# Performance work log

Hardware: AMD Instinct MI355X
Metric: run time of the kernel (lower is better)

The kernel has to match this reference:

```python
import jax, jax.numpy as jnp
import numpy as np

B, S, E, D, A = 32, 2048, 1024, 1024, 1024


def setup_inputs() -> dict:
    key = jax.random.key(0)
    k1, k2, k3, k4, k5, k6, k7, k8 = jax.random.split(key, 8)
    # Kaiming-uniform-ish init scales (values don't matter for correctness)
    def lin(kw, kb, fan_in, fan_out):
        bound = 1.0 / np.sqrt(fan_in)
        W = jax.random.uniform(kw, (fan_out, fan_in), minval=-bound, maxval=bound, dtype=jnp.float32)
        b = jax.random.uniform(kb, (fan_out,), minval=-bound, maxval=bound, dtype=jnp.float32)
        return W, b
    W_enc, b_enc = lin(k1, k2, E, A)
    W_dec, b_dec = lin(k3, k4, D, A)
    W_v, b_v = lin(k5, k6, A, 1)
    encoder_out = jax.random.normal(k7, (B, S, E), dtype=jnp.float32)
    decoder_hidden = jax.random.normal(k8, (B, D), dtype=jnp.float32)
    return {
        "encoder_out": encoder_out,
        "decoder_hidden": decoder_hidden,
        "W_enc": W_enc, "b_enc": b_enc,
        "W_dec": W_dec, "b_dec": b_dec,
        "W_v": W_v, "b_v": b_v,
    }


def reference(encoder_out, decoder_hidden, W_enc, b_enc, W_dec, b_dec, W_v, b_v):
    # encoder_proj: [B, S, A]
    encoder_proj = jnp.einsum('bse,ae->bsa', encoder_out, W_enc) + b_enc
    # decoder_proj: [B, 1, A]
    decoder_proj = (jnp.einsum('bd,ad->ba', decoder_hidden, W_dec) + b_dec)[:, None, :]
    # scores: [B, S] (V projects attention_dim -> 1)
    scores = jnp.einsum('bsa,a->bs', jnp.tanh(encoder_proj + decoder_proj), W_v[0]) + b_v[0]
    alpha = jax.nn.softmax(scores, axis=1)  # [B, S]
    context = jnp.einsum('bse,bs->be', encoder_out, alpha)  # [B, E]
    return (context, alpha)
```

## Files before the change

### kernel.cpp

```cpp
#include <hip/hip_runtime.h>

typedef unsigned short ushort_t;
typedef __attribute__((ext_vector_type(8))) short short8;
typedef __attribute__((ext_vector_type(4))) float f32x4;
typedef __attribute__((ext_vector_type(4))) unsigned int u32x4;


__device__ __forceinline__ ushort_t f2bf(float f) {
    unsigned u = __builtin_bit_cast(unsigned, f);
    u += 0x7fffu + ((u >> 16) & 1u);
    return (ushort_t)(u >> 16);
}

__device__ __forceinline__ unsigned pkbf(float a, float b) {
    unsigned r;
    asm("v_cvt_pk_bf16_f32 %0, %1, %2" : "=v"(r) : "v"(a), "v"(b));
    return r;
}

__device__ __forceinline__ float tanh_fast(float x) {
    float e = __expf(2.0f * x);
    float r = __builtin_amdgcn_rcpf(e + 1.0f);
    return __builtin_fmaf(-2.0f, r, 1.0f);
}

__device__ __forceinline__ void gld16(const ushort_t* g, ushort_t* lds) {
    __builtin_amdgcn_global_load_lds(
        (const __attribute__((address_space(1))) unsigned int*)g,
        (__attribute__((address_space(3))) unsigned int*)lds, 16, 0, 0);
}


__global__ __launch_bounds__(256) void k_prep(const float* __restrict__ Wenc,
                                              const float* __restrict__ dh,
                                              const float* __restrict__ Wd,
                                              const float* __restrict__ bd,
                                              const float* __restrict__ be,
                                              ushort_t* __restrict__ wencB,
                                              float* __restrict__ dproj,
                                              float4* __restrict__ scores4) {
    const int bx = blockIdx.x;
    const int t = threadIdx.x;
    if (bx < 256) {
        int idx = bx * 256 + t;
#pragma unroll
        for (int r = 0; r < 4; ++r) {
            int i = idx + r * 65536;
            float4 v = ((const float4*)Wenc)[i];
            ushort4 o;
            o.x = f2bf(v.x); o.y = f2bf(v.y); o.z = f2bf(v.z); o.w = f2bf(v.w);
            ((ushort4*)wencB)[i] = o;
        }
        if (idx < 16384) scores4[idx] = (float4){0.f, 0.f, 0.f, 0.f};
    } else {
        int wid = (bx - 256) * 4 + (t >> 6);
        int lane = t & 63;
        int a = wid & 1023, b = wid >> 10;
        const float4* x = (const float4*)(dh + (size_t)b * 1024);
        const float4* wrow = (const float4*)(Wd + (size_t)a * 1024);
        float s = 0.f;
#pragma unroll
        for (int it = 0; it < 4; ++it) {
            int c = it * 64 + lane;
            float4 xv = x[c], wv = wrow[c];
            s += xv.x * wv.x + xv.y * wv.y + xv.z * wv.z + xv.w * wv.w;
        }
#pragma unroll
        for (int o = 1; o < 64; o <<= 1) s += __shfl_xor(s, o, 64);
        if (lane == 0) dproj[b * 1024 + a] = s + bd[a] + be[a];
    }
}


__global__ __launch_bounds__(256, 2) void k_gemm_scores(const float* __restrict__ A,
                                                        const ushort_t* __restrict__ Bm,
                                                        const float* __restrict__ dproj,
                                                        const float* __restrict__ Wv,
                                                        float* __restrict__ scores) {
    __shared__ __align__(16) ushort_t At[256 * 64];
    __shared__ __align__(16) ushort_t Bt[128 * 64];

    const int tid = threadIdx.x;
    const int lane = tid & 63;
    const int w = tid >> 6;
    const int wm = w >> 1, wn = w & 1;

    const int blk = blockIdx.x;
    const int q2 = blk >> 3;
    const int blkN = q2 & 7;
    const int blkM = (blk & 7) + ((q2 >> 3) << 3);
    const long long arow0 = (long long)blkM * 256;
    const int brow0 = blkN * 128;

    const int sr = lane >> 3;
    const int sgrp = lane & 7;
    const int c8s = sgrp ^ sr;

    const int q = lane >> 4;
    const int ml = lane & 15;

    const float4* ga = (const float4*)(A + (size_t)(arow0 + w * 64 + sr) * 1024) + sgrp * 2;
    const ushort_t* gb = Bm + (size_t)(brow0 + w * 32 + sr) * 1024 + c8s * 8;
    const int wls = sr * 64 + (c8s << 3);

    f32x4 acc[8][4];
#pragma unroll
    for (int i = 0; i < 8; ++i)
#pragma unroll
        for (int jj = 0; jj < 4; ++jj) acc[i][jj] = (f32x4){0.f, 0.f, 0.f, 0.f};

    for (int k0 = 0; k0 < 1024; k0 += 64) {
        float4 p0[4], p1[4];
#pragma unroll
        for (int j = 0; j < 4; ++j) { p0[j] = ga[j * 2048]; p1[j] = ga[j * 2048 + 1]; }
        __syncthreads();
#pragma unroll
        for (int j = 0; j < 4; ++j)
            gld16(gb + j * 8192, &Bt[(w * 4 + j) * 512]);
#pragma unroll
        for (int j = 0; j < 4; ++j) {
            u32x4 o;
            o.x = pkbf(p0[j].x, p0[j].y); o.y = pkbf(p0[j].z, p0[j].w);
            o.z = pkbf(p1[j].x, p1[j].y); o.w = pkbf(p1[j].z, p1[j].w);
            *(u32x4*)&At[(w * 8 + j) * 512 + wls] = o;
        }
#pragma unroll
        for (int j = 4; j < 8; ++j) {
            float4 v0 = ga[j * 2048], v1 = ga[j * 2048 + 1];
            u32x4 o;
            o.x = pkbf(v0.x, v0.y); o.y = pkbf(v0.z, v0.w);
            o.z = pkbf(v1.x, v1.y); o.w = pkbf(v1.z, v1.w);
            *(u32x4*)&At[(w * 8 + j) * 512 + wls] = o;
        }
        ga += 16; gb += 64;
        __builtin_amdgcn_s_waitcnt(0);
        __syncthreads();

#pragma unroll
        for (int kk = 0; kk < 2; ++kk) {
            const int kb = kk * 4;
            const int slot = (kb + q) ^ (ml & 7);
            short8 af[8], bfr[4];
#pragma unroll
            for (int i = 0; i < 8; ++i) {
                int row = wm * 128 + i * 16 + ml;
                af[i] = *(const short8*)&At[row * 64 + slot * 8];
            }
#pragma unroll
            for (int jj = 0; jj < 4; ++jj) {
                int col = wn * 64 + jj * 16 + ml;
                bfr[jj] = *(const short8*)&Bt[col * 64 + slot * 8];
            }
#pragma unroll
            for (int i = 0; i < 8; ++i)
#pragma unroll
                for (int jj = 0; jj < 4; ++jj)
                    acc[i][jj] = __builtin_amdgcn_mfma_f32_16x16x32_bf16(
                        af[i], bfr[jj], acc[i][jj], 0, 0, 0);
        }
    }

    const int bb = blkM >> 3;
    float dp[4], wv[4];
#pragma unroll
    for (int jj = 0; jj < 4; ++jj) {
        int a = blkN * 128 + wn * 64 + jj * 16 + ml;
        dp[jj] = dproj[bb * 1024 + a];
        wv[jj] = Wv[a];
    }
#pragma unroll
    for (int i = 0; i < 8; ++i) {
        float rs[4] = {0.f, 0.f, 0.f, 0.f};
#pragma unroll
        for (int jj = 0; jj < 4; ++jj) {
            f32x4 v = acc[i][jj];
            rs[0] += wv[jj] * tanh_fast(v.x + dp[jj]);
            rs[1] += wv[jj] * tanh_fast(v.y + dp[jj]);
            rs[2] += wv[jj] * tanh_fast(v.z + dp[jj]);
            rs[3] += wv[jj] * tanh_fast(v.w + dp[jj]);
        }
#pragma unroll
        for (int r = 0; r < 4; ++r)
#pragma unroll
            for (int o = 1; o < 16; o <<= 1) rs[r] += __shfl_xor(rs[r], o, 64);
        if (ml == 0) {
            long long m0 = arow0 + wm * 128 + i * 16 + q * 4;
            atomicAdd(&scores[m0 + 0], rs[0]);
            atomicAdd(&scores[m0 + 1], rs[1]);
            atomicAdd(&scores[m0 + 2], rs[2]);
            atomicAdd(&scores[m0 + 3], rs[3]);
        }
    }
}


__global__ __launch_bounds__(256) void k_softmax(const float* __restrict__ scores,
                                                 float* __restrict__ alpha) {
    const int b = blockIdx.x, t = threadIdx.x;
    const int lane = t & 63, w = t >> 6;
    __shared__ float red[4];
    float v[8];
#pragma unroll
    for (int j = 0; j < 8; ++j) v[j] = scores[b * 2048 + j * 256 + t];
    float mx = v[0];
#pragma unroll
    for (int j = 1; j < 8; ++j) mx = fmaxf(mx, v[j]);
#pragma unroll
    for (int o = 1; o < 64; o <<= 1) mx = fmaxf(mx, __shfl_xor(mx, o, 64));
    if (lane == 0) red[w] = mx;
    __syncthreads();
    mx = fmaxf(fmaxf(red[0], red[1]), fmaxf(red[2], red[3]));
    float s = 0.f;
#pragma unroll
    for (int j = 0; j < 8; ++j) { v[j] = __expf(v[j] - mx); s += v[j]; }
#pragma unroll
    for (int o = 1; o < 64; o <<= 1) s += __shfl_xor(s, o, 64);
    __syncthreads();
    if (lane == 0) red[w] = s;
    __syncthreads();
    s = red[0] + red[1] + red[2] + red[3];
    float inv = 1.0f / s;
#pragma unroll
    for (int j = 0; j < 8; ++j) alpha[b * 2048 + j * 256 + t] = v[j] * inv;
}


__global__ __launch_bounds__(512) void k_context(const float* __restrict__ enc,
                                                 const float* __restrict__ alpha,
                                                 float* __restrict__ out) {
    const int b = blockIdx.x, ec = blockIdx.y;
    const int t = threadIdx.x;
    const int l = t & 31, g = t >> 5;
    __shared__ float al[2048];
    __shared__ f32x4 part[16][33];
    for (int j = t; j < 2048; j += 512) al[j] = alpha[b * 2048 + j];
    __syncthreads();
    const float4* ep = (const float4*)enc + ((size_t)b * 2048 + g) * 256 + ec * 32 + l;
    f32x4 acc = (f32x4){0.f, 0.f, 0.f, 0.f};
#pragma unroll 8
    for (int it = 0; it < 128; ++it) {
        float4 v = ep[(size_t)it * 4096];
        float a = al[g + it * 16];
        acc.x += a * v.x;
        acc.y += a * v.y;
        acc.z += a * v.z;
        acc.w += a * v.w;
    }
    part[g][l] = acc;
    __syncthreads();
    if (t < 32) {
        f32x4 s = part[0][t];
#pragma unroll
        for (int gg = 1; gg < 16; ++gg) {
            f32x4 p = part[gg][t];
            s.x += p.x; s.y += p.y; s.z += p.z; s.w += p.w;
        }
        *(float4*)(out + (size_t)b * 1024 + ec * 128 + t * 4) =
            (float4){s.x, s.y, s.z, s.w};
    }
}


extern "C" void kernel_launch(void* const* d_in, const int* in_sizes, int n_in,
                              void* d_out, int out_size, void* d_ws, size_t ws_size,
                              hipStream_t stream) {
    const float* enc  = (const float*)d_in[0];
    const float* dh   = (const float*)d_in[1];
    const float* Wenc = (const float*)d_in[2];
    const float* benc = (const float*)d_in[3];
    const float* Wdec = (const float*)d_in[4];
    const float* bdec = (const float*)d_in[5];
    const float* Wv   = (const float*)d_in[6];
    float* out = (float*)d_out;

    char* ws = (char*)d_ws;
    ushort_t* wencB = (ushort_t*)ws;
    float* dproj    = (float*)(ws + 2097152ull);
    float* scores   = (float*)(ws + 2097152ull + 131072ull);

    k_prep<<<8448, 256, 0, stream>>>(Wenc, dh, Wdec, bdec, benc,
                                     wencB, dproj, (float4*)scores);
    k_gemm_scores<<<2048, 256, 0, stream>>>(enc, wencB, dproj, Wv, scores);
    k_softmax<<<32, 256, 0, stream>>>(scores, out + 32768);
    k_context<<<dim3(32, 8), 512, 0, stream>>>(enc, out + 32768, out);
}
```

Measured before the change: 608.5 us.

## Software-pipeline GEMM global loads with double-buffered B tile and fuse softmax into context

The GEMM main loop now prefetches the next K-slice of A (into registers) and B (into a second LDS buffer) before running the MFMAs on the current slice. The converted A tile is written to LDS only after the compute step, so global load latency overlaps with matrix math instead of sitting behind a wait at the start of each slice. Separately, the softmax kernel is folded into the context kernel, with each block recomputing the softmax for its batch row, which removes one launch and the alpha round-trip. The cost is more registers (16 float4 prefetch values), an extra B buffer in LDS that may lower occupancy, and softmax done redundantly by 8 blocks per batch.

```diff
diff --git a/kernel.cpp b/kernel.cpp
--- a/kernel.cpp
+++ b/kernel.cpp
@@ -78,7 +78,7 @@
                                                         const float* __restrict__ Wv,
                                                         float* __restrict__ scores) {
     __shared__ __align__(16) ushort_t At[256 * 64];
-    __shared__ __align__(16) ushort_t Bt[128 * 64];
+    __shared__ __align__(16) ushort_t Bt[2][128 * 64];
 
     const int tid = threadIdx.x;
     const int lane = tid & 63;
@@ -101,7 +101,7 @@
 
     const float4* ga = (const float4*)(A + (size_t)(arow0 + w * 64 + sr) * 1024) + sgrp * 2;
     const ushort_t* gb = Bm + (size_t)(brow0 + w * 32 + sr) * 1024 + c8s * 8;
-    const int wls = sr * 64 + (c8s << 3);
+    ushort_t* atw = &At[w * 8 * 512 + sr * 64 + (c8s << 3)];
 
     f32x4 acc[8][4];
 #pragma unroll
@@ -109,55 +109,63 @@
 #pragma unroll
         for (int jj = 0; jj < 4; ++jj) acc[i][jj] = (f32x4){0.f, 0.f, 0.f, 0.f};
 
+    float4 p[16];
+
+#pragma unroll
+    for (int j = 0; j < 8; ++j) { p[2 * j] = ga[j * 2048]; p[2 * j + 1] = ga[j * 2048 + 1]; }
+#pragma unroll
+    for (int j = 0; j < 4; ++j) gld16(gb + j * 8192, &Bt[0][(w * 4 + j) * 512]);
+    ga += 16; gb += 64;
+#pragma unroll
+    for (int j = 0; j < 8; ++j) {
+        u32x4 o;
+        o.x = pkbf(p[2 * j].x, p[2 * j].y);         o.y = pkbf(p[2 * j].z, p[2 * j].w);
+        o.z = pkbf(p[2 * j + 1].x, p[2 * j + 1].y); o.w = pkbf(p[2 * j + 1].z, p[2 * j + 1].w);
+        *(u32x4*)(atw + j * 512) = o;
+    }
+    __syncthreads();
+
     for (int k0 = 0; k0 < 1024; k0 += 64) {
-        float4 p0[4], p1[4];
-#pragma unroll
-        for (int j = 0; j < 4; ++j) { p0[j] = ga[j * 2048]; p1[j] = ga[j * 2048 + 1]; }
-        __syncthreads();
-#pragma unroll
-        for (int j = 0; j < 4; ++j)
-            gld16(gb + j * 8192, &Bt[(w * 4 + j) * 512]);
-#pragma unroll
-        for (int j = 0; j < 4; ++j) {
-            u32x4 o;
-            o.x = pkbf(p0[j].x, p0[j].y); o.y = pkbf(p0[j].z, p0[j].w);
-            o.z = pkbf(p1[j].x, p1[j].y); o.w = pkbf(p1[j].z, p1[j].w);
-            *(u32x4*)&At[(w * 8 + j) * 512 + wls] = o;
-        }
-#pragma unroll
-        for (int j = 4; j < 8; ++j) {
-            float4 v0 = ga[j * 2048], v1 = ga[j * 2048 + 1];
-            u32x4 o;
-            o.x = pkbf(v0.x, v0.y); o.y = pkbf(v0.z, v0.w);
-            o.z = pkbf(v1.x, v1.y); o.w = pkbf(v1.z, v1.w);
-            *(u32x4*)&At[(w * 8 + j) * 512 + wls] = o;
-        }
-        ga += 16; gb += 64;
-        __builtin_amdgcn_s_waitcnt(0);
-        __syncthreads();
-
+        const int cur = (k0 >> 6) & 1;
+        const bool more = k0 < 960;
+        if (more) {
+#pragma unroll
+            for (int j = 0; j < 8; ++j) { p[2 * j] = ga[j * 2048]; p[2 * j + 1] = ga[j * 2048 + 1]; }
+#pragma unroll
+            for (int j = 0; j < 4; ++j) gld16(gb + j * 8192, &Bt[cur ^ 1][(w * 4 + j) * 512]);
+            ga += 16; gb += 64;
+        }
 #pragma unroll
         for (int kk = 0; kk < 2; ++kk) {
             const int kb = kk * 4;
             const int slot = (kb + q) ^ (ml & 7);
-            short8 af[8], bfr[4];
+            short8 bfr[4];
+#pragma unroll
+            for (int jj = 0; jj < 4; ++jj) {
+                int col = wn * 64 + jj * 16 + ml;
+                bfr[jj] = *(const short8*)&Bt[cur][col * 64 + slot * 8];
+            }
 #pragma unroll
             for (int i = 0; i < 8; ++i) {
                 int row = wm * 128 + i * 16 + ml;
-                af[i] = *(const short8*)&At[row * 64 + slot * 8];
-            }
-#pragma unroll
-            for (int jj = 0; jj < 4; ++jj) {
-                int col = wn * 64 + jj * 16 + ml;
-                bfr[jj] = *(const short8*)&Bt[col * 64 + slot * 8];
-            }
-#pragma unroll
-            for (int i = 0; i < 8; ++i)
+                short8 af = *(const short8*)&At[row * 64 + slot * 8];
 #pragma unroll
                 for (int jj = 0; jj < 4; ++jj)
                     acc[i][jj] = __builtin_amdgcn_mfma_f32_16x16x32_bf16(
-                        af[i], bfr[jj], acc[i][jj], 0, 0, 0);
-        }
+                        af, bfr[jj], acc[i][jj], 0, 0, 0);
+            }
+        }
+        __syncthreads();
+        if (more) {
+#pragma unroll
+            for (int j = 0; j < 8; ++j) {
+                u32x4 o;
+                o.x = pkbf(p[2 * j].x, p[2 * j].y);         o.y = pkbf(p[2 * j].z, p[2 * j].w);
+                o.z = pkbf(p[2 * j + 1].x, p[2 * j + 1].y); o.w = pkbf(p[2 * j + 1].z, p[2 * j + 1].w);
+                *(u32x4*)(atw + j * 512) = o;
+            }
+        }
+        __syncthreads();
     }
 
     const int bb = blkM >> 3;
@@ -194,69 +202,65 @@
 }
 
 
-__global__ __launch_bounds__(256) void k_softmax(const float* __restrict__ scores,
-                                                 float* __restrict__ alpha) {
-    const int b = blockIdx.x, t = threadIdx.x;
-    const int lane = t & 63, w = t >> 6;
-    __shared__ float red[4];
-    float v[8];
-#pragma unroll
-    for (int j = 0; j < 8; ++j) v[j] = scores[b * 2048 + j * 256 + t];
-    float mx = v[0];
-#pragma unroll
-    for (int j = 1; j < 8; ++j) mx = fmaxf(mx, v[j]);
-#pragma unroll
-    for (int o = 1; o < 64; o <<= 1) mx = fmaxf(mx, __shfl_xor(mx, o, 64));
-    if (lane == 0) red[w] = mx;
-    __syncthreads();
-    mx = fmaxf(fmaxf(red[0], red[1]), fmaxf(red[2], red[3]));
-    float s = 0.f;
-#pragma unroll
-    for (int j = 0; j < 8; ++j) { v[j] = __expf(v[j] - mx); s += v[j]; }
-#pragma unroll
-    for (int o = 1; o < 64; o <<= 1) s += __shfl_xor(s, o, 64);
-    __syncthreads();
-    if (lane == 0) red[w] = s;
-    __syncthreads();
-    s = red[0] + red[1] + red[2] + red[3];
-    float inv = 1.0f / s;
-#pragma unroll
-    for (int j = 0; j < 8; ++j) alpha[b * 2048 + j * 256 + t] = v[j] * inv;
-}
-
-
-__global__ __launch_bounds__(512) void k_context(const float* __restrict__ enc,
-                                                 const float* __restrict__ alpha,
-                                                 float* __restrict__ out) {
+__global__ __launch_bounds__(512) void k_ctx(const float* __restrict__ enc,
+                                             const float* __restrict__ scores,
+                                             float* __restrict__ out) {
     const int b = blockIdx.x, ec = blockIdx.y;
     const int t = threadIdx.x;
     const int l = t & 31, g = t >> 5;
+    const int lane = t & 63, wv = t >> 6;
     __shared__ float al[2048];
+    __shared__ float red[8];
     __shared__ f32x4 part[16][33];
-    for (int j = t; j < 2048; j += 512) al[j] = alpha[b * 2048 + j];
-    __syncthreads();
+
+    float4 v = ((const float4*)scores)[b * 512 + t];
+    float mx = fmaxf(fmaxf(v.x, v.y), fmaxf(v.z, v.w));
+#pragma unroll
+    for (int o = 1; o < 64; o <<= 1) mx = fmaxf(mx, __shfl_xor(mx, o, 64));
+    if (lane == 0) red[wv] = mx;
+    __syncthreads();
+    mx = red[0];
+#pragma unroll
+    for (int j = 1; j < 8; ++j) mx = fmaxf(mx, red[j]);
+    float e0 = __expf(v.x - mx), e1 = __expf(v.y - mx);
+    float e2 = __expf(v.z - mx), e3 = __expf(v.w - mx);
+    float s = e0 + e1 + e2 + e3;
+#pragma unroll
+    for (int o = 1; o < 64; o <<= 1) s += __shfl_xor(s, o, 64);
+    __syncthreads();
+    if (lane == 0) red[wv] = s;
+    __syncthreads();
+    s = 0.f;
+#pragma unroll
+    for (int j = 0; j < 8; ++j) s += red[j];
+    float inv = 1.0f / s;
+    float4 a4 = (float4){e0 * inv, e1 * inv, e2 * inv, e3 * inv};
+    ((float4*)al)[t] = a4;
+    if (ec == 0) ((float4*)(out + 32768 + (size_t)b * 2048))[t] = a4;
+    __syncthreads();
+
     const float4* ep = (const float4*)enc + ((size_t)b * 2048 + g) * 256 + ec * 32 + l;
     f32x4 acc = (f32x4){0.f, 0.f, 0.f, 0.f};
 #pragma unroll 8
     for (int it = 0; it < 128; ++it) {
-        float4 v = ep[(size_t)it * 4096];
+        float4 vv = ep[(size_t)it * 4096];
         float a = al[g + it * 16];
-        acc.x += a * v.x;
-        acc.y += a * v.y;
-        acc.z += a * v.z;
-        acc.w += a * v.w;
+        acc.x += a * vv.x;
+        acc.y += a * vv.y;
+        acc.z += a * vv.z;
+        acc.w += a * vv.w;
     }
     part[g][l] = acc;
     __syncthreads();
     if (t < 32) {
-        f32x4 s = part[0][t];
+        f32x4 ss = part[0][t];
 #pragma unroll
         for (int gg = 1; gg < 16; ++gg) {
-            f32x4 p = part[gg][t];
-            s.x += p.x; s.y += p.y; s.z += p.z; s.w += p.w;
+            f32x4 pp = part[gg][t];
+            ss.x += pp.x; ss.y += pp.y; ss.z += pp.z; ss.w += pp.w;
         }
         *(float4*)(out + (size_t)b * 1024 + ec * 128 + t * 4) =
-            (float4){s.x, s.y, s.z, s.w};
+            (float4){ss.x, ss.y, ss.z, ss.w};
     }
 }
 
@@ -281,6 +285,5 @@
     k_prep<<<8448, 256, 0, stream>>>(Wenc, dh, Wdec, bdec, benc,
                                      wencB, dproj, (float4*)scores);
     k_gemm_scores<<<2048, 256, 0, stream>>>(enc, wencB, dproj, Wv, scores);
-    k_softmax<<<32, 256, 0, stream>>>(scores, out + 32768);
-    k_context<<<dim3(32, 8), 512, 0, stream>>>(enc, out + 32768, out);
-}
+    k_ctx<<<dim3(32, 8), 512, 0, stream>>>(enc, scores, out);
+}
```

Result: faster. 592.6 us (-2.6%).
